# Kernel tuning notes

Hardware: AMD Instinct MI355X
Metric: run time of the kernel (lower is better)

## Reference

```python
import jax, jax.numpy as jnp
import numpy as np

B = 1024
IN_FEATURES = 4096
OUT_FEATURES = 4096
TOP_K = 64  # both k_prev (input width) and output top_k in this config


def setup_inputs() -> dict:
    key = jax.random.key(0)
    k1, k2, k3, k4 = jax.random.split(key, 4)
    bound = 1.0 / np.sqrt(IN_FEATURES)
    return {
        "input": jax.random.normal(k1, (B, TOP_K), dtype=jnp.float32),
        "weight": jax.random.uniform(k2, (OUT_FEATURES, IN_FEATURES), dtype=jnp.float32, minval=-bound, maxval=bound),
        "bias": jax.random.uniform(k3, (OUT_FEATURES,), dtype=jnp.float32, minval=-bound, maxval=bound),
        "previously_selected_nodes": jax.random.randint(k4, (B, TOP_K), 0, IN_FEATURES, dtype=jnp.int64).astype(jnp.int32),
    }


def reference(input, weight, bias, previously_selected_nodes):
    # Gather selected input-dim columns of weight per sample:
    # weight: (O, I), idx: (B, K) -> w_sel: (B, K, O)
    w_sel = jnp.take(weight.T, previously_selected_nodes, axis=0)
    # Batched matvec: (B, K, O) x (B, K) -> (B, O), plus bias
    result = jnp.einsum("bko,bk->bo", w_sel, input) + bias
    # Top-k selection over out_features, keep values and indices
    values, selected_nodes = jax.lax.top_k(result, TOP_K)
    return values, selected_nodes
```

## Files before the change

### kernel.cpp

```cpp
#include <hip/hip_runtime.h>
#include <stdint.h>

#define B_N 1024
#define K_N 64
#define O_N 4096
#define I_N 4096

typedef float nvec4 __attribute__((ext_vector_type(4)));

__global__ __launch_bounds__(256) void xpose_small(
    const float* __restrict__ x, const float* __restrict__ idxf,
    float* __restrict__ xT, float* __restrict__ idxTf) {
  __shared__ float tile[64][65];
  const int t = threadIdx.x;
  const int which = blockIdx.x >> 4;
  const int b0 = (blockIdx.x & 15) * 64;
  const float* src = which ? idxf : x;
  float* dst = which ? idxTf : xT;
  {
    const int r = t & 63;
    const int q0 = t >> 6;
#pragma unroll
    for (int jj = 0; jj < 4; ++jj) {
      const int q = q0 + 4 * jj;
      const float4 v = *(const float4*)(src + (size_t)(b0 + r) * K_N + 4 * q);
      tile[r][4 * q + 0] = v.x;
      tile[r][4 * q + 1] = v.y;
      tile[r][4 * q + 2] = v.z;
      tile[r][4 * q + 3] = v.w;
    }
  }
  __syncthreads();
  {
    const int kk = t & 63;
    const int q0 = t >> 6;
#pragma unroll
    for (int jj = 0; jj < 4; ++jj) {
      const int qb = q0 + 4 * jj;
      float4 v;
      v.x = tile[4 * qb + 0][kk];
      v.y = tile[4 * qb + 1][kk];
      v.z = tile[4 * qb + 2][kk];
      v.w = tile[4 * qb + 3][kk];
      *(float4*)(dst + (size_t)kk * B_N + b0 + 4 * qb) = v;
    }
  }
}

__global__ __launch_bounds__(1024, 4) void gemv_lds(
    const float* __restrict__ W, const float* __restrict__ xT,
    const int* __restrict__ idxT, const float* __restrict__ bias,
    float* __restrict__ res) {
  __shared__ float4 Wi[I_N];
  const int t = threadIdx.x;
  const int o0 = blockIdx.x * 4;

  {
    const int i0 = 4 * t;
    const nvec4 r0 = __builtin_nontemporal_load(
        (const nvec4*)(W + (size_t)(o0 + 0) * I_N + i0));
    const nvec4 r1 = __builtin_nontemporal_load(
        (const nvec4*)(W + (size_t)(o0 + 1) * I_N + i0));
    const nvec4 r2 = __builtin_nontemporal_load(
        (const nvec4*)(W + (size_t)(o0 + 2) * I_N + i0));
    const nvec4 r3 = __builtin_nontemporal_load(
        (const nvec4*)(W + (size_t)(o0 + 3) * I_N + i0));
    Wi[i0 + 0] = make_float4(r0.x, r1.x, r2.x, r3.x);
    Wi[i0 + 1] = make_float4(r0.y, r1.y, r2.y, r3.y);
    Wi[i0 + 2] = make_float4(r0.z, r1.z, r2.z, r3.z);
    Wi[i0 + 3] = make_float4(r0.w, r1.w, r2.w, r3.w);
  }
  __syncthreads();

  const int b = t;
  const float4 bv = *(const float4*)(bias + o0);
  float4 a = make_float4(0.f, 0.f, 0.f, 0.f);
  float xr[4];
  int ir[4];
#pragma unroll
  for (int d = 0; d < 4; ++d) {
    xr[d] = xT[d * B_N + b];
    ir[d] = idxT[d * B_N + b];
  }
#pragma unroll
  for (int k = 0; k < K_N; ++k) {
    const float xk = xr[k & 3];
    const int i = ir[k & 3];
    if (k + 4 < K_N) {
      xr[k & 3] = xT[(k + 4) * B_N + b];
      ir[k & 3] = idxT[(k + 4) * B_N + b];
    }
    const float4 w = Wi[i];
    a.x = __fadd_rn(a.x, __fmul_rn(xk, w.x));
    a.y = __fadd_rn(a.y, __fmul_rn(xk, w.y));
    a.z = __fadd_rn(a.z, __fmul_rn(xk, w.z));
    a.w = __fadd_rn(a.w, __fmul_rn(xk, w.w));
  }
  a.x = __fadd_rn(a.x, bv.x);
  a.y = __fadd_rn(a.y, bv.y);
  a.z = __fadd_rn(a.z, bv.z);
  a.w = __fadd_rn(a.w, bv.w);
  *(float4*)(res + (size_t)b * O_N + o0) = a;
}

__global__ __launch_bounds__(256) void topk_phase(
    const float* __restrict__ res, float* __restrict__ out) {
  __shared__ __align__(16) unsigned int hist[256];
  __shared__ unsigned int hist4[4 * 257];
  __shared__ unsigned int sel_u[64];
  __shared__ int sel_i[64];
  __shared__ int eqlist[128];
  __shared__ unsigned int s_cntgt, s_cnteq;
  __shared__ unsigned int s_remaining, s_prefix;

  const int t = threadIdx.x;
  const int b = blockIdx.x;
  const int w = t >> 6;

  hist[t] = 0u;
#pragma unroll
  for (int j = 0; j < 5; ++j) {
    const int z = t + 256 * j;
    if (z < 4 * 257) hist4[z] = 0u;
  }
  if (t == 0) {
    s_remaining = 64u;
    s_prefix = 0u;
    s_cntgt = 0u;
    s_cnteq = 0u;
  }

  unsigned int myu[16];
#pragma unroll
  for (int jf = 0; jf < 4; ++jf) {
    const float4 v =
        *(const float4*)(res + (size_t)b * O_N + 1024 * jf + 4 * t);
    const float fv[4] = {v.x, v.y, v.z, v.w};
#pragma unroll
    for (int c = 0; c < 4; ++c) {
      const unsigned int s = __float_as_uint(fv[c]);
      myu[jf * 4 + c] = (s & 0x80000000u) ? ~s : (s | 0x80000000u);
    }
  }
  __syncthreads();

  for (int round = 3; round >= 0; --round) {
    const int shift = round * 8;
    const unsigned int pfx = s_prefix;
    const unsigned int rem = s_remaining;
    if (round == 3) {
#pragma unroll
      for (int j = 0; j < 16; ++j)
        atomicAdd(&hist4[w * 257 + (myu[j] >> 24)], 1u);
    } else {
      const unsigned int himask = 0xFFFFFFFFu << (shift + 8);
#pragma unroll
      for (int j = 0; j < 16; ++j) {
        if ((myu[j] & himask) == (pfx & himask))
          atomicAdd(&hist[(myu[j] >> shift) & 255u], 1u);
      }
    }
    __syncthreads();
    if (t < 64) {
      uint4 h;
      if (round == 3) {
        h.x = hist4[0 * 257 + 4 * t + 0] + hist4[1 * 257 + 4 * t + 0] +
              hist4[2 * 257 + 4 * t + 0] + hist4[3 * 257 + 4 * t + 0];
        h.y = hist4[0 * 257 + 4 * t + 1] + hist4[1 * 257 + 4 * t + 1] +
              hist4[2 * 257 + 4 * t + 1] + hist4[3 * 257 + 4 * t + 1];
        h.z = hist4[0 * 257 + 4 * t + 2] + hist4[1 * 257 + 4 * t + 2] +
              hist4[2 * 257 + 4 * t + 2] + hist4[3 * 257 + 4 * t + 2];
        h.w = hist4[0 * 257 + 4 * t + 3] + hist4[1 * 257 + 4 * t + 3] +
              hist4[2 * 257 + 4 * t + 3] + hist4[3 * 257 + 4 * t + 3];
      } else {
        h = *(const uint4*)&hist[4 * t];
      }
      unsigned int s0 = h.x + h.y + h.z + h.w;
      unsigned int run = s0;
#pragma unroll
      for (int off = 1; off < 64; off <<= 1) {
        const unsigned int v = __shfl_down(run, off, 64);
        if (t + off < 64) run += v;
      }
      const unsigned int above = run - s0;
      unsigned int cge[4], cgt[4];
      cgt[3] = above;
      cge[3] = above + h.w;
      cgt[2] = cge[3];
      cge[2] = cge[3] + h.z;
      cgt[1] = cge[2];
      cge[1] = cge[2] + h.y;
      cgt[0] = cge[1];
      cge[0] = cge[1] + h.x;
#pragma unroll
      for (int j = 0; j < 4; ++j) {
        if (cge[j] >= rem && cgt[j] < rem) {
          s_prefix = pfx | ((unsigned int)(4 * t + j) << shift);
          s_remaining = rem - cgt[j];
        }
      }
      *(uint4*)&hist[4 * t] = make_uint4(0u, 0u, 0u, 0u);
    }
    __syncthreads();
  }
  const unsigned int ustar = s_prefix;

#pragma unroll
  for (int j = 0; j < 16; ++j) {
    const unsigned int u = myu[j];
    const int oi = 4 * t + (j & 3) + 1024 * (j >> 2);
    if (u > ustar) {
      unsigned int p = atomicAdd(&s_cntgt, 1u);
      sel_u[p] = u;
      sel_i[p] = oi;
    } else if (u == ustar) {
      unsigned int p = atomicAdd(&s_cnteq, 1u);
      if (p < 128u) eqlist[p] = oi;
    }
  }
  __syncthreads();

  if (t == 0 && s_cnteq > 1u) {
    int n = (int)(s_cnteq < 128u ? s_cnteq : 128u);
    for (int a = 1; a < n; ++a) {
      int v = eqlist[a];
      int c = a;
      while (c > 0 && eqlist[c - 1] > v) {
        eqlist[c] = eqlist[c - 1];
        --c;
      }
      eqlist[c] = v;
    }
  }
  __syncthreads();

  if (t < 64) {
    const int n_gt = (int)s_cntgt;
    unsigned int u;
    int oi;
    if (t < n_gt) {
      u = sel_u[t];
      oi = sel_i[t];
    } else {
      u = ustar;
      oi = eqlist[t - n_gt];
    }
    unsigned long long key =
        ((unsigned long long)(~u) << 32) | (unsigned int)oi;
    for (int kk = 2; kk <= 64; kk <<= 1) {
      for (int jj = kk >> 1; jj > 0; jj >>= 1) {
        unsigned long long partner = __shfl_xor(key, jj, 64);
        const bool up = ((t & kk) == 0);
        const bool lower = ((t & jj) == 0);
        unsigned long long mn = key < partner ? key : partner;
        unsigned long long mx = key < partner ? partner : key;
        key = (up == lower) ? mn : mx;
      }
    }
    const unsigned int su = ~(unsigned int)(key >> 32);
    const int so = (int)(key & 0xFFFFFFFFu);
    const float f = (su & 0x80000000u) ? __uint_as_float(su ^ 0x80000000u)
                                       : __uint_as_float(~su);
    out[b * 64 + t] = f;
    out[B_N * 64 + b * 64 + t] = (float)so;
  }
}

__global__ __launch_bounds__(256) void selgemv_topk(
    const float* __restrict__ x, const float* __restrict__ Wsrc,
    const float* __restrict__ bias, const int* __restrict__ idx,
    float* __restrict__ out) {
  __shared__ float sx[K_N];
  __shared__ int si[K_N];
  __shared__ float svals[O_N];
  __shared__ unsigned int hist[256];
  __shared__ unsigned int scan[256];
  __shared__ unsigned int sel_u[64];
  __shared__ int sel_i[64];
  __shared__ int eqlist[128];
  __shared__ unsigned int s_T, s_ngt, s_cntgt, s_cnteq;
  __shared__ unsigned int s_remaining, s_prefix;

  const int t = threadIdx.x;
  const int b = blockIdx.x;

  if (t < K_N) {
    sx[t] = x[b * K_N + t];
    si[t] = idx[b * K_N + t];
  }
  if (t == 0) {
    s_remaining = 64u;
    s_prefix = 0u;
    s_cntgt = 0u;
    s_cnteq = 0u;
  }
  __syncthreads();

  float acc[16];
#pragma unroll
  for (int j = 0; j < 16; ++j) acc[j] = 0.0f;

  for (int k = 0; k < K_N; ++k) {
    const float xk = sx[k];
    const int ik = si[k];
#pragma unroll
    for (int j = 0; j < 4; ++j) {
      int o0 = (j * 256 + t) * 4;
#pragma unroll
      for (int c = 0; c < 4; ++c) {
        float w = Wsrc[(size_t)(o0 + c) * I_N + ik];
        acc[4 * j + c] = __fadd_rn(acc[4 * j + c], __fmul_rn(xk, w));
      }
    }
  }

#pragma unroll
  for (int j = 0; j < 4; ++j) {
    int g = j * 256 + t;
    float4 bb = ((const float4*)bias)[g];
    float4 r;
    r.x = __fadd_rn(acc[4 * j + 0], bb.x);
    r.y = __fadd_rn(acc[4 * j + 1], bb.y);
    r.z = __fadd_rn(acc[4 * j + 2], bb.z);
    r.w = __fadd_rn(acc[4 * j + 3], bb.w);
    ((float4*)svals)[g] = r;
  }
  __syncthreads();

  unsigned int myu[16];
#pragma unroll
  for (int j = 0; j < 16; ++j) {
    float f = svals[t + 256 * j];
    unsigned int s = __float_as_uint(f);
    myu[j] = (s & 0x80000000u) ? ~s : (s | 0x80000000u);
  }

  for (int round = 3; round >= 0; --round) {
    const int shift = round * 8;
    hist[t] = 0u;
    __syncthreads();
    const unsigned int pfx = s_prefix;
    const unsigned int rem = s_remaining;
    const unsigned int himask =
        (round == 3) ? 0u : (0xFFFFFFFFu << (shift + 8));
#pragma unroll
    for (int j = 0; j < 16; ++j) {
      if ((myu[j] & himask) == (pfx & himask))
        atomicAdd(&hist[(myu[j] >> shift) & 255u], 1u);
    }
    __syncthreads();
    scan[t] = hist[t];
    __syncthreads();
    for (int off = 1; off < 256; off <<= 1) {
      unsigned int v = (t + off < 256) ? scan[t + off] : 0u;
      __syncthreads();
      scan[t] += v;
      __syncthreads();
    }
    const unsigned int c_ge = scan[t];
    const unsigned int c_gt = (t < 255) ? scan[t + 1] : 0u;
    if (c_ge >= rem && c_gt < rem) {
      s_T = (unsigned int)t;
      s_ngt = c_gt;
    }
    __syncthreads();
    if (t == 0) {
      s_prefix |= (s_T << shift);
      s_remaining -= s_ngt;
    }
    __syncthreads();
  }
  const unsigned int ustar = s_prefix;

#pragma unroll
  for (int j = 0; j < 16; ++j) {
    const unsigned int u = myu[j];
    if (u > ustar) {
      unsigned int p = atomicAdd(&s_cntgt, 1u);
      sel_u[p] = u;
      sel_i[p] = t + 256 * j;
    } else if (u == ustar) {
      unsigned int p = atomicAdd(&s_cnteq, 1u);
      if (p < 128u) eqlist[p] = t + 256 * j;
    }
  }
  __syncthreads();

  if (t == 0 && s_cnteq > 1u) {
    int n = (int)(s_cnteq < 128u ? s_cnteq : 128u);
    for (int a = 1; a < n; ++a) {
      int v = eqlist[a];
      int c = a;
      while (c > 0 && eqlist[c - 1] > v) {
        eqlist[c] = eqlist[c - 1];
        --c;
      }
      eqlist[c] = v;
    }
  }
  __syncthreads();

  if (t < 64) {
    const int n_gt = (int)s_cntgt;
    unsigned int u;
    int oi;
    if (t < n_gt) {
      u = sel_u[t];
      oi = sel_i[t];
    } else {
      u = ustar;
      oi = eqlist[t - n_gt];
    }
    unsigned long long key =
        ((unsigned long long)(~u) << 32) | (unsigned int)oi;
    for (int kk = 2; kk <= 64; kk <<= 1) {
      for (int jj = kk >> 1; jj > 0; jj >>= 1) {
        unsigned long long partner = __shfl_xor(key, jj, 64);
        const bool up = ((t & kk) == 0);
        const bool lower = ((t & jj) == 0);
        unsigned long long mn = key < partner ? key : partner;
        unsigned long long mx = key < partner ? partner : key;
        key = (up == lower) ? mn : mx;
      }
    }
    const unsigned int su = ~(unsigned int)(key >> 32);
    const int so = (int)(key & 0xFFFFFFFFu);
    const float f = (su & 0x80000000u) ? __uint_as_float(su ^ 0x80000000u)
                                       : __uint_as_float(~su);
    out[b * 64 + t] = f;
    out[B_N * 64 + b * 64 + t] = (float)so;
  }
}

extern "C" void kernel_launch(void* const* d_in, const int* in_sizes, int n_in,
                              void* d_out, int out_size, void* d_ws,
                              size_t ws_size, hipStream_t stream) {
  const float* x = (const float*)d_in[0];
  const float* W = (const float*)d_in[1];
  const float* bias = (const float*)d_in[2];
  const int* idx = (const int*)d_in[3];
  float* out = (float*)d_out;

  const size_t xT_bytes = (size_t)K_N * B_N * sizeof(float);
  const size_t idxT_bytes = xT_bytes;
  const size_t res_bytes = (size_t)B_N * O_N * sizeof(float);

  if (ws_size >= xT_bytes + idxT_bytes + res_bytes) {
    float* xT = (float*)d_ws;
    float* idxTf = (float*)((char*)d_ws + xT_bytes);
    float* res = (float*)((char*)d_ws + xT_bytes + idxT_bytes);
    xpose_small<<<32, 256, 0, stream>>>(x, (const float*)idx, xT, idxTf);
    gemv_lds<<<O_N / 4, 1024, 0, stream>>>(W, xT, (const int*)idxTf, bias,
                                           res);
    topk_phase<<<B_N, 256, 0, stream>>>(res, out);
  } else {
    selgemv_topk<<<B_N, 256, 0, stream>>>(x, W, bias, idx, out);
  }
}
```

Measured before the change: 157.2 us.

## Stage two weight rows per block in LDS and loop over batch halves

The gathered-weight GEMV now stages two output rows per block (a 32KB float2 LDS tile) instead of four (64KB float4), using 512-thread blocks that each process two batch rows in sequence. The smaller LDS footprint and block size are meant to raise occupancy and allow more resident blocks per CU. In exchange the idx/x streams are reread twice as many times across blocks, each thread does more serial work, and the result writes become 8-byte rather than 16-byte stores.

```diff
diff --git a/kernel.cpp b/kernel.cpp
--- a/kernel.cpp
+++ b/kernel.cpp
@@ -47,60 +47,59 @@
   }
 }
 
-__global__ __launch_bounds__(1024, 4) void gemv_lds(
+__global__ __launch_bounds__(512, 8) void gemv_lds(
     const float* __restrict__ W, const float* __restrict__ xT,
     const int* __restrict__ idxT, const float* __restrict__ bias,
     float* __restrict__ res) {
-  __shared__ float4 Wi[I_N];
+  __shared__ float2 Wi[I_N];
   const int t = threadIdx.x;
-  const int o0 = blockIdx.x * 4;
+  const int o0 = blockIdx.x * 2;
 
   {
-    const int i0 = 4 * t;
-    const nvec4 r0 = __builtin_nontemporal_load(
+    const int i0 = 8 * t;
+    const nvec4 a0 = __builtin_nontemporal_load(
         (const nvec4*)(W + (size_t)(o0 + 0) * I_N + i0));
-    const nvec4 r1 = __builtin_nontemporal_load(
+    const nvec4 a1 = __builtin_nontemporal_load(
+        (const nvec4*)(W + (size_t)(o0 + 0) * I_N + i0 + 4));
+    const nvec4 b0 = __builtin_nontemporal_load(
         (const nvec4*)(W + (size_t)(o0 + 1) * I_N + i0));
-    const nvec4 r2 = __builtin_nontemporal_load(
-        (const nvec4*)(W + (size_t)(o0 + 2) * I_N + i0));
-    const nvec4 r3 = __builtin_nontemporal_load(
-        (const nvec4*)(W + (size_t)(o0 + 3) * I_N + i0));
-    Wi[i0 + 0] = make_float4(r0.x, r1.x, r2.x, r3.x);
-    Wi[i0 + 1] = make_float4(r0.y, r1.y, r2.y, r3.y);
-    Wi[i0 + 2] = make_float4(r0.z, r1.z, r2.z, r3.z);
-    Wi[i0 + 3] = make_float4(r0.w, r1.w, r2.w, r3.w);
-  }
-  __syncthreads();
-
-  const int b = t;
-  const float4 bv = *(const float4*)(bias + o0);
-  float4 a = make_float4(0.f, 0.f, 0.f, 0.f);
-  float xr[4];
-  int ir[4];
-#pragma unroll
-  for (int d = 0; d < 4; ++d) {
-    xr[d] = xT[d * B_N + b];
-    ir[d] = idxT[d * B_N + b];
-  }
-#pragma unroll
-  for (int k = 0; k < K_N; ++k) {
-    const float xk = xr[k & 3];
-    const int i = ir[k & 3];
-    if (k + 4 < K_N) {
-      xr[k & 3] = xT[(k + 4) * B_N + b];
-      ir[k & 3] = idxT[(k + 4) * B_N + b];
-    }
-    const float4 w = Wi[i];
-    a.x = __fadd_rn(a.x, __fmul_rn(xk, w.x));
-    a.y = __fadd_rn(a.y, __fmul_rn(xk, w.y));
-    a.z = __fadd_rn(a.z, __fmul_rn(xk, w.z));
-    a.w = __fadd_rn(a.w, __fmul_rn(xk, w.w));
-  }
-  a.x = __fadd_rn(a.x, bv.x);
-  a.y = __fadd_rn(a.y, bv.y);
-  a.z = __fadd_rn(a.z, bv.z);
-  a.w = __fadd_rn(a.w, bv.w);
-  *(float4*)(res + (size_t)b * O_N + o0) = a;
+    const nvec4 b1 = __builtin_nontemporal_load(
+        (const nvec4*)(W + (size_t)(o0 + 1) * I_N + i0 + 4));
+    *(float4*)&Wi[i0 + 0] = make_float4(a0.x, b0.x, a0.y, b0.y);
+    *(float4*)&Wi[i0 + 2] = make_float4(a0.z, b0.z, a0.w, b0.w);
+    *(float4*)&Wi[i0 + 4] = make_float4(a1.x, b1.x, a1.y, b1.y);
+    *(float4*)&Wi[i0 + 6] = make_float4(a1.z, b1.z, a1.w, b1.w);
+  }
+  __syncthreads();
+
+  const float2 bv = *(const float2*)(bias + o0);
+#pragma unroll
+  for (int c = 0; c < 2; ++c) {
+    const int b = c * 512 + t;
+    float2 a = make_float2(0.f, 0.f);
+    float xr[4];
+    int ir[4];
+#pragma unroll
+    for (int d = 0; d < 4; ++d) {
+      xr[d] = xT[d * B_N + b];
+      ir[d] = idxT[d * B_N + b];
+    }
+#pragma unroll
+    for (int k = 0; k < K_N; ++k) {
+      const float xk = xr[k & 3];
+      const int i = ir[k & 3];
+      if (k + 4 < K_N) {
+        xr[k & 3] = xT[(k + 4) * B_N + b];
+        ir[k & 3] = idxT[(k + 4) * B_N + b];
+      }
+      const float2 w = Wi[i];
+      a.x = __fadd_rn(a.x, __fmul_rn(xk, w.x));
+      a.y = __fadd_rn(a.y, __fmul_rn(xk, w.y));
+    }
+    a.x = __fadd_rn(a.x, bv.x);
+    a.y = __fadd_rn(a.y, bv.y);
+    *(float2*)(res + (size_t)b * O_N + o0) = a;
+  }
 }
 
 __global__ __launch_bounds__(256) void topk_phase(
@@ -450,8 +449,8 @@
     float* idxTf = (float*)((char*)d_ws + xT_bytes);
     float* res = (float*)((char*)d_ws + xT_bytes + idxT_bytes);
     xpose_small<<<32, 256, 0, stream>>>(x, (const float*)idx, xT, idxTf);
-    gemv_lds<<<O_N / 4, 1024, 0, stream>>>(W, xT, (const int*)idxTf, bias,
-                                           res);
+    gemv_lds<<<O_N / 2, 512, 0, stream>>>(W, xT, (const int*)idxTf, bias,
+                                          res);
     topk_phase<<<B_N, 256, 0, stream>>>(res, out);
   } else {
     selgemv_topk<<<B_N, 256, 0, stream>>>(x, W, bias, idx, out);
```

Result: slower. 203.2 us (+29.3%).
